# Kernel tuning notes

Measured on AMD Instinct MI355X. Metric: run time of the kernel, lower is better.

The kernel has to match this reference:

```python
import jax, jax.numpy as jnp
import numpy as np

IGNORE = -1.0e6  # masked-score fill value (applied BEFORE the /d_head scaling, as in torch)


def setup_inputs() -> dict:
    key = jax.random.key(0)
    ks = jax.random.split(key, 7)
    B, S, D, N, H = 1, 256, 512, 8, 64
    std = 0.02
    return {
        "normalized_resid_pre": jax.random.normal(ks[0], (B, S, D), jnp.float32),
        "W_K1": jax.random.normal(ks[1], (N, D, H), jnp.float32) * std,
        "W_K2": jax.random.normal(ks[2], (N, D, H), jnp.float32) * std,
        "W_Q": jax.random.normal(ks[3], (N, D, H), jnp.float32) * std,
        "W_V12": jax.random.normal(ks[4], (N, 2 * D, H), jnp.float32) * std,
        "W_O": jax.random.normal(ks[5], (N, H, D), jnp.float32) * std,
        "b_K1": jnp.zeros((N, H), jnp.float32),
        "b_K2": jnp.zeros((N, H), jnp.float32),
        "b_Q": jnp.zeros((N, H), jnp.float32),
        "b_V12": jnp.zeros((N, H), jnp.float32),
        "b_O": jnp.zeros((D,), jnp.float32),
    }


def reference(normalized_resid_pre, W_K1, W_K2, W_Q, W_V12, W_O,
              b_K1, b_K2, b_Q, b_V12, b_O):
    x = normalized_resid_pre
    B, S, D = x.shape
    N, _, H = W_K1.shape

    k1 = jnp.einsum('ndh,bpd->bpnh', W_K1, x) + b_K1
    k2 = jnp.einsum('ndh,bpd->bpnh', W_K2, x) + b_K2
    q = jnp.einsum('ndh,bpd->bpnh', W_Q, x) + b_Q

    # v[b,p,s,n,h] = W_V12[:, :D] @ x[b,p] + W_V12[:, D:] @ x[b,s] + b_V12
    # (equivalent to cat((v1, v2)) @ W_V12 without materializing the [b,p,s,2D] tensor)
    vA = jnp.einsum('ndh,bpd->bpnh', W_V12[:, :D, :], x)
    vB = jnp.einsum('ndh,bpd->bpnh', W_V12[:, D:, :], x)
    v = vA[:, :, None] + vB[:, None, :] + b_V12  # [b, p, s, n, h]
    v = v.reshape(B, S * S, N, H)                # [b, (p s), n, h]

    # cubic attention scores: [b, n, s, t, q]
    scores = jnp.einsum('bsnh,btnh,bqnh->bnstq', k1, k2, q)

    # causal mask (causal_attn=True, attn_eq=False, order_attn=True):
    # mask = (s >= q) | (t >= q) | (s >= t)
    i_s = jnp.arange(S)[:, None, None]
    i_t = jnp.arange(S)[None, :, None]
    i_q = jnp.arange(S)[None, None, :]
    mask = (i_s >= i_q) | (i_t >= i_q) | (i_s >= i_t)  # [S, S, S]
    scores = jnp.where(mask[None, None], IGNORE, scores)

    # rearrange 'b n s t q -> b n q (s t)', then scale by d_head and softmax
    scores = jnp.transpose(scores, (0, 1, 4, 2, 3)).reshape(B, N, S, S * S) / H
    attn = jax.nn.softmax(scores, axis=-1)       # [b, n, q, (s t)]

    z = jnp.einsum('bnql,blnh->bqnh', attn, v)
    out = jnp.einsum('bqnh,nhd->bqd', z, W_O) + b_O
    return out
```

## Files before the change

### kernel.cpp

```cpp
#include <hip/hip_runtime.h>

#define SS 256
#define DD 512
#define NN 8
#define HH 64

typedef __bf16 bf16x8 __attribute__((ext_vector_type(8)));
typedef __bf16 bf16x4 __attribute__((ext_vector_type(4)));
typedef float  floatx4 __attribute__((ext_vector_type(4)));

__global__ __launch_bounds__(256) void proj_kernel(
    const float* __restrict__ x,
    const float* __restrict__ WK1, const float* __restrict__ WK2,
    const float* __restrict__ WQ,  const float* __restrict__ WV12,
    const float* __restrict__ bK1, const float* __restrict__ bK2,
    const float* __restrict__ bQ,  const float* __restrict__ bO,
    float* __restrict__ K1b, float* __restrict__ Qb,
    __bf16* __restrict__ K2bf, __bf16* __restrict__ VAbf,
    __bf16* __restrict__ VBbf, float* __restrict__ outp)
{
    const int blk = blockIdx.x;
    const int m  = blk >> 6;
    const int tid  = threadIdx.x;

    __shared__ __bf16 xsh[32 * DD];

    if (m == 5) {
        const int idx = blk & 63;
        const int q = idx * 4 + (tid >> 6);
        const int d = (tid & 63) * 8;
        const float4 b0 = *(const float4*)(bO + d);
        const float4 b1 = *(const float4*)(bO + d + 4);
        *(float4*)(outp + q * DD + d)     = b0;
        *(float4*)(outp + q * DD + d + 4) = b1;
        return;
    }

    const int pt = blk & 7;
    const int n  = (blk >> 3) & 7;
    const int lane = tid & 63;
    const int wid  = tid >> 6;
    const int r15  = lane & 15;
    const int quad = lane >> 4;
    const int p0 = pt * 32;

    const float* W;
    if (m == 0)      W = WK1  + n * DD * HH;
    else if (m == 1) W = WK2  + n * DD * HH;
    else if (m == 2) W = WQ   + n * DD * HH;
    else if (m == 3) W = WV12 + n * 2 * DD * HH;
    else             W = WV12 + n * 2 * DD * HH + DD * HH;

    for (int it = 0; it < 8; ++it) {
        const int idx = tid + it * 256;
        const int row = idx >> 6;
        const int c8  = idx & 63;
        const float4 xa = *(const float4*)(x + (p0 + row) * DD + c8 * 8);
        const float4 xb = *(const float4*)(x + (p0 + row) * DD + c8 * 8 + 4);
        bf16x8 v;
        v[0]=(__bf16)xa.x; v[1]=(__bf16)xa.y; v[2]=(__bf16)xa.z; v[3]=(__bf16)xa.w;
        v[4]=(__bf16)xb.x; v[5]=(__bf16)xb.y; v[6]=(__bf16)xb.z; v[7]=(__bf16)xb.w;
        *(bf16x8*)&xsh[row * DD + ((c8 ^ (row & 7)) << 3)] = v;
    }
    __syncthreads();

    const int h0 = wid << 4;
    const int swz = r15 & 7;
    floatx4 C0 = {0.f,0.f,0.f,0.f}, C1 = {0.f,0.f,0.f,0.f};
    for (int kk = 0; kk < 16; ++kk) {
        const int c8 = (kk << 2) + quad;
        const bf16x8 A0 = *(const bf16x8*)&xsh[ r15       * DD + ((c8 ^ swz) << 3)];
        const bf16x8 A1 = *(const bf16x8*)&xsh[(16 + r15) * DD + ((c8 ^ swz) << 3)];
        const float* Wp = W + (kk * 32 + quad * 8) * HH + h0 + r15;
        bf16x8 Bv;
        #pragma unroll
        for (int j = 0; j < 8; ++j) Bv[j] = (__bf16)Wp[j * HH];
        C0 = __builtin_amdgcn_mfma_f32_16x16x32_bf16(A0, Bv, C0, 0, 0, 0);
        C1 = __builtin_amdgcn_mfma_f32_16x16x32_bf16(A1, Bv, C1, 0, 0, 0);
    }

    float bv = 0.f;
    if (m == 0)      bv = bK1[n * HH + h0 + r15];
    else if (m == 1) bv = bK2[n * HH + h0 + r15];
    else if (m == 2) bv = bQ[n * HH + h0 + r15];

    if (m == 1) {
        const int h = h0 + r15;
        const int c8 = h >> 3;
        #pragma unroll
        for (int i = 0; i < 4; ++i) {
            int p = p0 + quad * 4 + i;
            K2bf[(n * SS + p) * HH + ((c8 ^ (p & 7)) << 3) + (h & 7)] =
                (__bf16)(C0[i] + bv);
            p += 16;
            K2bf[(n * SS + p) * HH + ((c8 ^ (p & 7)) << 3) + (h & 7)] =
                (__bf16)(C1[i] + bv);
        }
    } else if (m >= 3) {
        __bf16* outb = (m == 3) ? VAbf : VBbf;
        #pragma unroll
        for (int i = 0; i < 4; ++i) {
            const int p = p0 + quad * 4 + i;
            outb[(n * SS + p) * HH + h0 + r15]      = (__bf16)C0[i];
            outb[(n * SS + p + 16) * HH + h0 + r15] = (__bf16)C1[i];
        }
    } else {
        float* outb = (m == 0) ? K1b : Qb;
        const float scale = (m == 2) ? (1.0f / 64.0f) : 1.0f;
        #pragma unroll
        for (int i = 0; i < 4; ++i) {
            const int p = p0 + quad * 4 + i;
            outb[(n * SS + p) * HH + h0 + r15]      = (C0[i] + bv) * scale;
            outb[(n * SS + p + 16) * HH + h0 + r15] = (C1[i] + bv) * scale;
        }
    }
}

__global__ __launch_bounds__(256, 3) void attn_kernel(
    const float* __restrict__ K1b, const __bf16* __restrict__ K2bf,
    const float* __restrict__ Qb,  const __bf16* __restrict__ VAbf,
    const __bf16* __restrict__ VBbf, const float* __restrict__ bV12,
    const float* __restrict__ WO, float* __restrict__ outp)
{
    const int n = blockIdx.x & 7;
    const int g = (int)(blockIdx.x >> 3);
    int qs4[4];
    qs4[0] = g; qs4[1] = 127 - g; qs4[2] = 128 + g; qs4[3] = 255 - g;
    const int qmax = qs4[3];

    const int tid  = threadIdx.x;
    const int lane = tid & 63;
    const int wid  = tid >> 6;
    const int r15  = lane & 15;
    const int quad = lane >> 4;

    __shared__ __bf16 K2sh[SS * HH];
    __shared__ float qsh[4][HH];
    __shared__ float a_lds[4][SS];
    __shared__ float c_lds[4][SS];
    __shared__ float zred[4][4][HH];
    __shared__ float red[4][4];

    {
        const __bf16* src = K2bf + (n << 8) * HH;
        for (int it = 0; it < 8; ++it) {
            const int idx = tid + it * 256;
            *(bf16x8*)&K2sh[idx * 8] = *(const bf16x8*)&src[idx * 8];
        }
        if (tid < 64) {
            const int qi = tid >> 4, c = tid & 15;
            const float4 qv = *(const float4*)(Qb + ((n << 8) + qs4[qi]) * HH + c * 4);
            *(float4*)&qsh[qi][c * 4] = qv;
        }
        #pragma unroll
        for (int qi = 0; qi < 4; ++qi) {
            const float init = (qs4[qi] < 2) ? (1.0f / SS) : 0.f;
            a_lds[qi][tid] = init;
            c_lds[qi][tid] = init;
        }
    }
    __syncthreads();

    #pragma unroll
    for (int j = 0; j < 4; ++j) {
        int strip;
        if (j == 0) strip = wid;
        else if (j == 1) strip = 7 - wid;
        else if (j == 2) strip = 8 + wid;
        else strip = 15 - wid;
        const int s0 = strip << 4;
        if (s0 + 2 > qmax) continue;

        const float* k1p = K1b + ((n << 8) + s0 + r15) * HH;
        const float4 ka = *(const float4*)(k1p + quad * 8);
        const float4 kb = *(const float4*)(k1p + quad * 8 + 4);
        const float4 kc = *(const float4*)(k1p + 32 + quad * 8);
        const float4 kd = *(const float4*)(k1p + 32 + quad * 8 + 4);

        bf16x8 a0q[4], a1q[4];
        #pragma unroll
        for (int qi = 0; qi < 4; ++qi) {
            const float4 qa = *(const float4*)&qsh[qi][quad * 8];
            const float4 qb_ = *(const float4*)&qsh[qi][quad * 8 + 4];
            const float4 qc = *(const float4*)&qsh[qi][32 + quad * 8];
            const float4 qd = *(const float4*)&qsh[qi][32 + quad * 8 + 4];
            a0q[qi][0] = (__bf16)(ka.x * qa.x); a0q[qi][1] = (__bf16)(ka.y * qa.y);
            a0q[qi][2] = (__bf16)(ka.z * qa.z); a0q[qi][3] = (__bf16)(ka.w * qa.w);
            a0q[qi][4] = (__bf16)(kb.x * qb_.x); a0q[qi][5] = (__bf16)(kb.y * qb_.y);
            a0q[qi][6] = (__bf16)(kb.z * qb_.z); a0q[qi][7] = (__bf16)(kb.w * qb_.w);
            a1q[qi][0] = (__bf16)(kc.x * qc.x); a1q[qi][1] = (__bf16)(kc.y * qc.y);
            a1q[qi][2] = (__bf16)(kc.z * qc.z); a1q[qi][3] = (__bf16)(kc.w * qc.w);
            a1q[qi][4] = (__bf16)(kd.x * qd.x); a1q[qi][5] = (__bf16)(kd.y * qd.y);
            a1q[qi][6] = (__bf16)(kd.z * qd.z); a1q[qi][7] = (__bf16)(kd.w * qd.w);
        }

        float rowAcc[4][4] = {};
        const int swz = r15 & 7;
        for (int t0 = s0; t0 < qmax; t0 += 16) {
            const __bf16* K2row = &K2sh[(t0 + r15) * HH];
            const bf16x8 b0 = *(const bf16x8*)&K2row[((quad    ) ^ swz) << 3];
            const bf16x8 b1 = *(const bf16x8*)&K2row[((quad + 4) ^ swz) << 3];
            #pragma unroll
            for (int qi = 0; qi < 4; ++qi) {
                const int qv = qs4[qi];
                if (t0 >= qv || s0 + 2 > qv) continue;
                floatx4 C = {0.f, 0.f, 0.f, 0.f};
                C = __builtin_amdgcn_mfma_f32_16x16x32_bf16(a0q[qi], b0, C, 0, 0, 0);
                C = __builtin_amdgcn_mfma_f32_16x16x32_bf16(a1q[qi], b1, C, 0, 0, 0);

                float e[4];
                if (t0 >= s0 + 16 && t0 + 16 <= qv) {
                    #pragma unroll
                    for (int i = 0; i < 4; ++i) e[i] = __expf(C[i]);
                } else {
                    const int t = t0 + r15;
                    #pragma unroll
                    for (int i = 0; i < 4; ++i) {
                        const int s = s0 + quad * 4 + i;
                        e[i] = (s < t && t < qv) ? __expf(C[i]) : 0.f;
                    }
                }
                #pragma unroll
                for (int i = 0; i < 4; ++i) rowAcc[qi][i] += e[i];

                float cs = (e[0] + e[1]) + (e[2] + e[3]);
                cs += __shfl_xor(cs, 16, 64);
                cs += __shfl_xor(cs, 32, 64);
                if (lane < 16) atomicAdd(&c_lds[qi][t0 + r15], cs);
            }
        }
        #pragma unroll
        for (int qi = 0; qi < 4; ++qi) {
            if (s0 + 2 > qs4[qi]) continue;
            #pragma unroll
            for (int i = 0; i < 4; ++i) {
                rowAcc[qi][i] += __shfl_xor(rowAcc[qi][i], 1, 64);
                rowAcc[qi][i] += __shfl_xor(rowAcc[qi][i], 2, 64);
                rowAcc[qi][i] += __shfl_xor(rowAcc[qi][i], 4, 64);
                rowAcc[qi][i] += __shfl_xor(rowAcc[qi][i], 8, 64);
            }
            if (r15 == 0) {
                #pragma unroll
                for (int i = 0; i < 4; ++i)
                    a_lds[qi][s0 + quad * 4 + i] = rowAcc[qi][i];
            }
        }
    }
    __syncthreads();

    #pragma unroll
    for (int qi = 0; qi < 4; ++qi) {
        float v = a_lds[qi][tid];
        #pragma unroll
        for (int off = 32; off >= 1; off >>= 1) v += __shfl_xor(v, off, 64);
        if (lane == 0) red[qi][wid] = v;
    }
    __syncthreads();
    float invZ[4];
    #pragma unroll
    for (int qi = 0; qi < 4; ++qi)
        invZ[qi] = 1.0f / (red[qi][0] + red[qi][1] + red[qi][2] + red[qi][3]);

    {
        const int h = lane;
        const int gg = wid;
        const __bf16* VAp = VAbf + ((n << 8) + (gg << 6)) * HH + h;
        const __bf16* VBp = VBbf + ((n << 8) + (gg << 6)) * HH + h;
        float acc[4] = {0.f, 0.f, 0.f, 0.f};
        for (int i = 0; i < 64; ++i) {
            const float va = (float)VAp[i * HH];
            const float vb = (float)VBp[i * HH];
            const int si = (gg << 6) + i;
            #pragma unroll
            for (int qi = 0; qi < 4; ++qi)
                acc[qi] = fmaf(a_lds[qi][si], va,
                          fmaf(c_lds[qi][si], vb, acc[qi]));
        }
        #pragma unroll
        for (int qi = 0; qi < 4; ++qi) zred[qi][gg][h] = acc[qi];
    }
    __syncthreads();
    {
        const int qi = wid;
        const int h = lane;
        qsh[qi][h] = (zred[qi][0][h] + zred[qi][1][h] +
                      zred[qi][2][h] + zred[qi][3][h]) * invZ[qi]
                   + bV12[n * HH + h];
    }
    __syncthreads();

    {
        const int qi = wid;
        const int q  = qs4[qi];
        const int d0 = lane * 4;
        const float* WOp = WO + (n * HH) * DD;
        floatx4 acc0 = {0.f,0.f,0.f,0.f}, acc1 = {0.f,0.f,0.f,0.f};
        for (int h = 0; h < HH; ++h) {
            const float zv = qsh[qi][h];
            const float4 w0 = *(const float4*)(WOp + h * DD + d0);
            const float4 w1 = *(const float4*)(WOp + h * DD + d0 + 256);
            acc0[0] = fmaf(zv, w0.x, acc0[0]); acc0[1] = fmaf(zv, w0.y, acc0[1]);
            acc0[2] = fmaf(zv, w0.z, acc0[2]); acc0[3] = fmaf(zv, w0.w, acc0[3]);
            acc1[0] = fmaf(zv, w1.x, acc1[0]); acc1[1] = fmaf(zv, w1.y, acc1[1]);
            acc1[2] = fmaf(zv, w1.z, acc1[2]); acc1[3] = fmaf(zv, w1.w, acc1[3]);
        }
        float* op = outp + q * DD;
        #pragma unroll
        for (int i = 0; i < 4; ++i) {
            atomicAdd(op + d0 + i,       acc0[i]);
            atomicAdd(op + d0 + 256 + i, acc1[i]);
        }
    }
}

extern "C" void kernel_launch(void* const* d_in, const int* in_sizes, int n_in,
                              void* d_out, int out_size, void* d_ws, size_t ws_size,
                              hipStream_t stream)
{
    const float* x    = (const float*)d_in[0];
    const float* WK1  = (const float*)d_in[1];
    const float* WK2  = (const float*)d_in[2];
    const float* WQ   = (const float*)d_in[3];
    const float* WV12 = (const float*)d_in[4];
    const float* WO   = (const float*)d_in[5];
    const float* bK1  = (const float*)d_in[6];
    const float* bK2  = (const float*)d_in[7];
    const float* bQ   = (const float*)d_in[8];
    const float* bV12 = (const float*)d_in[9];
    const float* bO   = (const float*)d_in[10];
    float* out = (float*)d_out;

    float* ws  = (float*)d_ws;
    const int T = NN * SS * HH;
    float*  K1b  = ws + 0 * T;
    float*  Qb   = ws + 1 * T;
    __bf16* b16  = (__bf16*)(ws + 2 * T);
    __bf16* K2bf = b16 + 0 * T;
    __bf16* VAbf = b16 + 1 * T;
    __bf16* VBbf = b16 + 2 * T;

    proj_kernel<<<384, 256, 0, stream>>>(x, WK1, WK2, WQ, WV12,
                                         bK1, bK2, bQ, bO,
                                         K1b, Qb, K2bf, VAbf, VBbf, out);
    attn_kernel<<<512, 256, 0, stream>>>(K1b, K2bf, Qb, VAbf, VBbf, bV12,
                                         WO, out);
}
```

Measured before the change: 127.4 us.

## Split attention work to two queries per block and double the grid

Each attention block now handles two balanced query rows (g and 255-g) instead of four, and the grid grows from 512 to 1024 blocks. Launch bounds are raised to four blocks per SM. The output projection is remapped so all four waves share the W_O loads across both queries. This gives more parallelism and lighter per-block register and LDS use, but each block still loads the full K2 tile into shared memory, so K2 staging traffic per query doubles.

```diff
diff --git a/kernel.cpp b/kernel.cpp
--- a/kernel.cpp
+++ b/kernel.cpp
@@ -116,7 +116,7 @@
     }
 }
 
-__global__ __launch_bounds__(256, 3) void attn_kernel(
+__global__ __launch_bounds__(256, 4) void attn_kernel(
     const float* __restrict__ K1b, const __bf16* __restrict__ K2bf,
     const float* __restrict__ Qb,  const __bf16* __restrict__ VAbf,
     const __bf16* __restrict__ VBbf, const float* __restrict__ bV12,
@@ -124,9 +124,9 @@
 {
     const int n = blockIdx.x & 7;
     const int g = (int)(blockIdx.x >> 3);
-    int qs4[4];
-    qs4[0] = g; qs4[1] = 127 - g; qs4[2] = 128 + g; qs4[3] = 255 - g;
-    const int qmax = qs4[3];
+    int qs2[2];
+    qs2[0] = g; qs2[1] = 255 - g;
+    const int qmax = qs2[1];
 
     const int tid  = threadIdx.x;
     const int lane = tid & 63;
@@ -135,11 +135,11 @@
     const int quad = lane >> 4;
 
     __shared__ __bf16 K2sh[SS * HH];
-    __shared__ float qsh[4][HH];
-    __shared__ float a_lds[4][SS];
-    __shared__ float c_lds[4][SS];
-    __shared__ float zred[4][4][HH];
-    __shared__ float red[4][4];
+    __shared__ float qsh[2][HH];
+    __shared__ float a_lds[2][SS];
+    __shared__ float c_lds[2][SS];
+    __shared__ float zred[2][4][HH];
+    __shared__ float red[2][4];
 
     {
         const __bf16* src = K2bf + (n << 8) * HH;
@@ -147,14 +147,14 @@
             const int idx = tid + it * 256;
             *(bf16x8*)&K2sh[idx * 8] = *(const bf16x8*)&src[idx * 8];
         }
-        if (tid < 64) {
+        if (tid < 32) {
             const int qi = tid >> 4, c = tid & 15;
-            const float4 qv = *(const float4*)(Qb + ((n << 8) + qs4[qi]) * HH + c * 4);
+            const float4 qv = *(const float4*)(Qb + ((n << 8) + qs2[qi]) * HH + c * 4);
             *(float4*)&qsh[qi][c * 4] = qv;
         }
         #pragma unroll
-        for (int qi = 0; qi < 4; ++qi) {
-            const float init = (qs4[qi] < 2) ? (1.0f / SS) : 0.f;
+        for (int qi = 0; qi < 2; ++qi) {
+            const float init = (qs2[qi] < 2) ? (1.0f / SS) : 0.f;
             a_lds[qi][tid] = init;
             c_lds[qi][tid] = init;
         }
@@ -177,9 +177,9 @@
         const float4 kc = *(const float4*)(k1p + 32 + quad * 8);
         const float4 kd = *(const float4*)(k1p + 32 + quad * 8 + 4);
 
-        bf16x8 a0q[4], a1q[4];
-        #pragma unroll
-        for (int qi = 0; qi < 4; ++qi) {
+        bf16x8 a0q[2], a1q[2];
+        #pragma unroll
+        for (int qi = 0; qi < 2; ++qi) {
             const float4 qa = *(const float4*)&qsh[qi][quad * 8];
             const float4 qb_ = *(const float4*)&qsh[qi][quad * 8 + 4];
             const float4 qc = *(const float4*)&qsh[qi][32 + quad * 8];
@@ -194,15 +194,15 @@
             a1q[qi][6] = (__bf16)(kd.z * qd.z); a1q[qi][7] = (__bf16)(kd.w * qd.w);
         }
 
-        float rowAcc[4][4] = {};
+        float rowAcc[2][4] = {};
         const int swz = r15 & 7;
         for (int t0 = s0; t0 < qmax; t0 += 16) {
             const __bf16* K2row = &K2sh[(t0 + r15) * HH];
             const bf16x8 b0 = *(const bf16x8*)&K2row[((quad    ) ^ swz) << 3];
             const bf16x8 b1 = *(const bf16x8*)&K2row[((quad + 4) ^ swz) << 3];
             #pragma unroll
-            for (int qi = 0; qi < 4; ++qi) {
-                const int qv = qs4[qi];
+            for (int qi = 0; qi < 2; ++qi) {
+                const int qv = qs2[qi];
                 if (t0 >= qv || s0 + 2 > qv) continue;
                 floatx4 C = {0.f, 0.f, 0.f, 0.f};
                 C = __builtin_amdgcn_mfma_f32_16x16x32_bf16(a0q[qi], b0, C, 0, 0, 0);
@@ -230,8 +230,8 @@
             }
         }
         #pragma unroll
-        for (int qi = 0; qi < 4; ++qi) {
-            if (s0 + 2 > qs4[qi]) continue;
+        for (int qi = 0; qi < 2; ++qi) {
+            if (s0 + 2 > qs2[qi]) continue;
             #pragma unroll
             for (int i = 0; i < 4; ++i) {
                 rowAcc[qi][i] += __shfl_xor(rowAcc[qi][i], 1, 64);
@@ -249,16 +249,16 @@
     __syncthreads();
 
     #pragma unroll
-    for (int qi = 0; qi < 4; ++qi) {
+    for (int qi = 0; qi < 2; ++qi) {
         float v = a_lds[qi][tid];
         #pragma unroll
         for (int off = 32; off >= 1; off >>= 1) v += __shfl_xor(v, off, 64);
         if (lane == 0) red[qi][wid] = v;
     }
     __syncthreads();
-    float invZ[4];
+    float invZ[2];
     #pragma unroll
-    for (int qi = 0; qi < 4; ++qi)
+    for (int qi = 0; qi < 2; ++qi)
         invZ[qi] = 1.0f / (red[qi][0] + red[qi][1] + red[qi][2] + red[qi][3]);
 
     {
@@ -266,23 +266,23 @@
         const int gg = wid;
         const __bf16* VAp = VAbf + ((n << 8) + (gg << 6)) * HH + h;
         const __bf16* VBp = VBbf + ((n << 8) + (gg << 6)) * HH + h;
-        float acc[4] = {0.f, 0.f, 0.f, 0.f};
+        float acc[2] = {0.f, 0.f};
         for (int i = 0; i < 64; ++i) {
             const float va = (float)VAp[i * HH];
             const float vb = (float)VBp[i * HH];
             const int si = (gg << 6) + i;
             #pragma unroll
-            for (int qi = 0; qi < 4; ++qi)
+            for (int qi = 0; qi < 2; ++qi)
                 acc[qi] = fmaf(a_lds[qi][si], va,
                           fmaf(c_lds[qi][si], vb, acc[qi]));
         }
         #pragma unroll
-        for (int qi = 0; qi < 4; ++qi) zred[qi][gg][h] = acc[qi];
-    }
-    __syncthreads();
-    {
-        const int qi = wid;
-        const int h = lane;
+        for (int qi = 0; qi < 2; ++qi) zred[qi][gg][h] = acc[qi];
+    }
+    __syncthreads();
+    if (tid < 128) {
+        const int qi = tid >> 6;
+        const int h = tid & 63;
         qsh[qi][h] = (zred[qi][0][h] + zred[qi][1][h] +
                       zred[qi][2][h] + zred[qi][3][h]) * invZ[qi]
                    + bV12[n * HH + h];
@@ -290,26 +290,22 @@
     __syncthreads();
 
     {
-        const int qi = wid;
-        const int q  = qs4[qi];
-        const int d0 = lane * 4;
+        const int d0 = (wid << 7) + lane * 2;
         const float* WOp = WO + (n * HH) * DD;
-        floatx4 acc0 = {0.f,0.f,0.f,0.f}, acc1 = {0.f,0.f,0.f,0.f};
+        float2 acc0 = {0.f, 0.f}, acc1 = {0.f, 0.f};
         for (int h = 0; h < HH; ++h) {
-            const float zv = qsh[qi][h];
-            const float4 w0 = *(const float4*)(WOp + h * DD + d0);
-            const float4 w1 = *(const float4*)(WOp + h * DD + d0 + 256);
-            acc0[0] = fmaf(zv, w0.x, acc0[0]); acc0[1] = fmaf(zv, w0.y, acc0[1]);
-            acc0[2] = fmaf(zv, w0.z, acc0[2]); acc0[3] = fmaf(zv, w0.w, acc0[3]);
-            acc1[0] = fmaf(zv, w1.x, acc1[0]); acc1[1] = fmaf(zv, w1.y, acc1[1]);
-            acc1[2] = fmaf(zv, w1.z, acc1[2]); acc1[3] = fmaf(zv, w1.w, acc1[3]);
-        }
-        float* op = outp + q * DD;
-        #pragma unroll
-        for (int i = 0; i < 4; ++i) {
-            atomicAdd(op + d0 + i,       acc0[i]);
-            atomicAdd(op + d0 + 256 + i, acc1[i]);
-        }
+            const float2 w = *(const float2*)(WOp + h * DD + d0);
+            const float z0 = qsh[0][h];
+            const float z1 = qsh[1][h];
+            acc0.x = fmaf(z0, w.x, acc0.x); acc0.y = fmaf(z0, w.y, acc0.y);
+            acc1.x = fmaf(z1, w.x, acc1.x); acc1.y = fmaf(z1, w.y, acc1.y);
+        }
+        float* op0 = outp + qs2[0] * DD + d0;
+        float* op1 = outp + qs2[1] * DD + d0;
+        atomicAdd(op0,     acc0.x);
+        atomicAdd(op0 + 1, acc0.y);
+        atomicAdd(op1,     acc1.x);
+        atomicAdd(op1 + 1, acc1.y);
     }
 }
 
@@ -342,6 +338,6 @@
     proj_kernel<<<384, 256, 0, stream>>>(x, WK1, WK2, WQ, WV12,
                                          bK1, bK2, bQ, bO,
                                          K1b, Qb, K2bf, VAbf, VBbf, out);
-    attn_kernel<<<512, 256, 0, stream>>>(K1b, K2bf, Qb, VAbf, VBbf, bV12,
-                                         WO, out);
+    attn_kernel<<<1024, 256, 0, stream>>>(K1b, K2bf, Qb, VAbf, VBbf, bV12,
+                                          WO, out);
 }
```

Result: faster. 118.7 us (-6.8%).
